# Optimization experiments

Hardware: AMD Instinct MI355X
Metric: run time of the kernel (lower is better)

The kernel has to match this reference:

```python
import jax, jax.numpy as jnp
from jax import lax
import numpy as np

BALANCE = 1.0  # polynomial kernel: (conv(x,w)+b + BALANCE)**POWER
POWER = 2


def _conv(x, w, b, stride, pad):
    y = lax.conv_general_dilated(
        x, w, window_strides=(stride, stride),
        padding=[(pad, pad), (pad, pad)],
        dimension_numbers=('NCHW', 'OIHW', 'NCHW'))
    return y + b[None, :, None, None]


def kerv2d(x, w, b, stride, pad):
    # PolyKervNets degree-2 polynomial kervolution
    y = _conv(x, w, b, stride, pad) + BALANCE
    return y * y  # (.)**2


def avgpool3s2(x):
    s = lax.reduce_window(x, 0.0, lax.add, (1, 1, 3, 3), (1, 1, 2, 2), 'VALID')
    return s * (1.0 / 9.0)


def setup_inputs() -> dict:
    key = jax.random.key(0)
    ks = jax.random.split(key, 17)
    sc = 0.01  # small init so repeated squaring stays numerically sane
    d = {}
    d['x'] = jax.random.normal(ks[0], (64, 3, 227, 227), jnp.float32)
    d['w1'] = jax.random.normal(ks[1], (96, 3, 11, 11), jnp.float32) * sc
    d['b1'] = jnp.zeros((96,), jnp.float32)
    d['w2'] = jax.random.normal(ks[2], (256, 96, 5, 5), jnp.float32) * sc
    d['b2'] = jnp.zeros((256,), jnp.float32)
    d['w3'] = jax.random.normal(ks[3], (384, 256, 3, 3), jnp.float32) * sc
    d['b3'] = jnp.zeros((384,), jnp.float32)
    d['w4'] = jax.random.normal(ks[4], (384, 384, 3, 3), jnp.float32) * sc
    d['b4'] = jnp.zeros((384,), jnp.float32)
    d['w5'] = jax.random.normal(ks[5], (256, 384, 3, 3), jnp.float32) * sc
    d['b5'] = jnp.zeros((256,), jnp.float32)
    d['fw1'] = jax.random.normal(ks[6], (9216, 4096), jnp.float32) * sc
    d['fb1'] = jnp.zeros((4096,), jnp.float32)
    d['fw2'] = jax.random.normal(ks[7], (4096, 4096), jnp.float32) * sc
    d['fb2'] = jnp.zeros((4096,), jnp.float32)
    d['fw3'] = jax.random.normal(ks[8], (4096, 1000), jnp.float32) * sc
    d['fb3'] = jnp.zeros((1000,), jnp.float32)
    return d


def reference(x, w1, b1, w2, b2, w3, b3, w4, b4, w5, b5,
              fw1, fb1, fw2, fb2, fw3, fb3):
    x = kerv2d(x, w1, b1, stride=4, pad=0)   # [B,96,55,55]
    x = avgpool3s2(x)                        # [B,96,27,27]
    x = kerv2d(x, w2, b2, stride=1, pad=2)   # [B,256,27,27]
    x = avgpool3s2(x)                        # [B,256,13,13]
    x = kerv2d(x, w3, b3, stride=1, pad=1)   # [B,384,13,13]
    x = kerv2d(x, w4, b4, stride=1, pad=1)   # [B,384,13,13]
    x = kerv2d(x, w5, b5, stride=1, pad=1)   # [B,256,13,13]
    x = avgpool3s2(x)                        # [B,256,6,6]
    x = x.reshape(x.shape[0], -1)            # [B,9216]
    x = x @ fw1 + fb1
    x = x @ fw2 + fb2
    x = x @ fw3 + fb3
    return x
```

## Files before the change

kernel.cpp:

```cpp
#include <hip/hip_runtime.h>


typedef _Float16 f16;
typedef _Float16 f16x8 __attribute__((ext_vector_type(8)));
typedef float    f32x4 __attribute__((ext_vector_type(4)));

#define CDIV(a,b) (((a)+(b)-1)/(b))
#define SWZ(row,g) ((g) ^ (((row) >> 2) & 3))

template<int C,int H,int W,int OC,int R,int S,int PAD,int STRIDE,int OH,int OW,
         int KRUN,int BM,int BN>
__global__ __launch_bounds__(256)
void conv_mfma(const f16* __restrict__ in, const f16* __restrict__ wt,
               const float* __restrict__ bias, f16* __restrict__ out)
{
    constexpr int KTOT = (KRUN > 0) ? (R * KRUN) : (C * R * S);
    constexpr int KP   = (KTOT + 31) & ~31;
    static_assert(KRUN > 0 || (C % 32) == 0, "vector path requires C % 32 == 0");
    constexpr int OHW  = OH * OW;
    constexpr int NTOT = 64 * OHW;
    constexpr int AM   = BM / 32;
    constexpr int AN   = BN / 32;
    constexpr int AU   = BM * 4 / 256;
    constexpr int BU   = BN * 4 / 256;

    __shared__ __align__(16) f16 As[BM * 32];
    __shared__ __align__(16) f16 Bs[BN * 32];

    const int t   = threadIdx.x;
    const int n0  = blockIdx.x * BN;
    const int oc0 = blockIdx.y * BM;

    int a_lds[AU]; bool a_ok[AU]; const f16* aptr[AU];
    #pragma unroll
    for (int i = 0; i < AU; ++i) {
        const int u   = t + i * 256;
        const int row = u >> 2;
        const int g   = u & 3;
        a_lds[i] = row * 32 + SWZ(row, g) * 8;
        a_ok[i]  = (oc0 + row) < OC;
        const int rowc = a_ok[i] ? (oc0 + row) : 0;
        aptr[i] = wt + (size_t)rowc * KP + g * 8;
    }
    int b_lds[BU], b_g[BU], b_img[BU], b_oy[BU], b_ox[BU]; bool b_ok[BU];
    #pragma unroll
    for (int i = 0; i < BU; ++i) {
        const int u   = t + i * 256;
        const int row = u >> 2;
        b_g[i]   = u & 3;
        b_lds[i] = row * 32 + SWZ(row, b_g[i]) * 8;
        const int n   = n0 + row;
        b_ok[i]       = n < NTOT;
        const int ncl = b_ok[i] ? n : 0;
        b_img[i] = ncl / OHW;
        const int rem = ncl - b_img[i] * OHW;
        b_oy[i]  = rem / OW;
        b_ox[i]  = rem - b_oy[i] * OW;
    }

    const int wv = t >> 6;
    const int wm = (wv >> 1) * (BM / 2);
    const int wn = (wv & 1) * (BN / 2);
    const int l  = t & 63;
    const int il = l & 15;
    const int q  = l >> 4;

    f32x4 acc[AM][AN];
    #pragma unroll
    for (int i = 0; i < AM; ++i)
        #pragma unroll
        for (int j = 0; j < AN; ++j)
            acc[i][j] = (f32x4){0.f, 0.f, 0.f, 0.f};

    int4 aReg[AU], bReg[BU];

    auto loadA = [&](int kc) {
        #pragma unroll
        for (int i = 0; i < AU; ++i) {
            int4 v = {0, 0, 0, 0};
            if (a_ok[i]) v = *(const int4*)(aptr[i] + kc);
            aReg[i] = v;
        }
    };

    const f16* bcur[BU]; bool bval[BU];
    auto setRS = [&](int r, int s) {
        if constexpr (KRUN == 0) {
            #pragma unroll
            for (int i = 0; i < BU; ++i) {
                const int iy = b_oy[i] * STRIDE + r - PAD;
                const int ix = b_ox[i] * STRIDE + s - PAD;
                bval[i] = b_ok[i] && iy >= 0 && iy < H && ix >= 0 && ix < W;
                bcur[i] = in + ((size_t)(b_img[i] * H + iy) * W + ix) * C + b_g[i] * 8;
            }
        }
    };
    auto loadBv = [&](int ccoff) {
        #pragma unroll
        for (int i = 0; i < BU; ++i) {
            int4 v = {0, 0, 0, 0};
            if (bval[i]) v = *(const int4*)(bcur[i] + ccoff);
            bReg[i] = v;
        }
    };
    auto loadB1 = [&](int kc) {
        if constexpr (KRUN > 0) {
            #pragma unroll
            for (int i = 0; i < BU; ++i) {
                const int k8 = kc + b_g[i] * 8;
                const int r  = k8 / KRUN;
                const int j0 = k8 - r * KRUN;
                int4 v = {0, 0, 0, 0};
                if (b_ok[i] && k8 < KTOT) {
                    const f16* p = in + ((size_t)(b_img[i] * H + b_oy[i] * STRIDE + r) * W
                                         + b_ox[i] * STRIDE) * C + j0;
                    const int2 lo = *(const int2*)p;
                    const int2 hi = *(const int2*)(p + 4);
                    v.x = lo.x; v.y = lo.y; v.z = hi.x; v.w = hi.y;
                }
                bReg[i] = v;
            }
        }
    };

    loadA(0);
    if constexpr (KRUN > 0) { loadB1(0); }
    else                    { setRS(0, 0); loadBv(0); }

    int rn = 0, sn = 0, ccn = 0;

    for (int kc = 0; kc < KP; kc += 32) {
        #pragma unroll
        for (int i = 0; i < AU; ++i) *(int4*)&As[a_lds[i]] = aReg[i];
        #pragma unroll
        for (int i = 0; i < BU; ++i) *(int4*)&Bs[b_lds[i]] = bReg[i];
        __syncthreads();

        if (kc + 32 < KP) {
            loadA(kc + 32);
            if constexpr (KRUN > 0) {
                loadB1(kc + 32);
            } else {
                ccn += 32;
                if (ccn == C) {
                    ccn = 0;
                    if (++sn == S) { sn = 0; ++rn; }
                    setRS(rn, sn);
                }
                loadBv(ccn);
            }
        }

        f16x8 af[AM], bf[AN];
        #pragma unroll
        for (int mi = 0; mi < AM; ++mi) {
            const int row = wm + mi * 16 + il;
            af[mi] = *(const f16x8*)&As[row * 32 + SWZ(row, q) * 8];
        }
        #pragma unroll
        for (int ni = 0; ni < AN; ++ni) {
            const int row = wn + ni * 16 + il;
            bf[ni] = *(const f16x8*)&Bs[row * 32 + SWZ(row, q) * 8];
        }
        #pragma unroll
        for (int mi = 0; mi < AM; ++mi)
            #pragma unroll
            for (int ni = 0; ni < AN; ++ni)
                acc[mi][ni] = __builtin_amdgcn_mfma_f32_16x16x32_f16(
                    af[mi], bf[ni], acc[mi][ni], 0, 0, 0);
        __syncthreads();
    }

    #pragma unroll
    for (int mi = 0; mi < AM; ++mi) {
        const int ocb = oc0 + wm + mi * 16 + q * 4;
        if (ocb >= OC) continue;
        const float4 bb = *(const float4*)(bias + ocb);
        const float b4[4] = {bb.x + 1.f, bb.y + 1.f, bb.z + 1.f, bb.w + 1.f};
        #pragma unroll
        for (int ni = 0; ni < AN; ++ni) {
            const int nn = n0 + wn + ni * 16 + il;
            if (nn >= NTOT) continue;
            const f32x4 v = acc[mi][ni];
            union { f16 h[4]; uint2 u; } cv;
            const float vv[4] = {v.x, v.y, v.z, v.w};
            #pragma unroll
            for (int rr = 0; rr < 4; ++rr) {
                const float y = vv[rr] + b4[rr];
                cv.h[rr] = (f16)(y * y);
            }
            *(uint2*)(out + (size_t)nn * OC + ocb) = cv.u;
        }
    }
}

template<bool TAIL>
__global__ __launch_bounds__(256)
void fc_mfma2(const f16* __restrict__ X, const float* __restrict__ Wm,
              float* __restrict__ P, int N, int Npad, int K, int kchunk)
{
    __shared__ __align__(16) f16 Xs[64 * 32];
    __shared__ __align__(16) f16 Ws[256 * 32];

    const int t  = threadIdx.x;
    const int n0 = blockIdx.x * 256;
    const int s  = blockIdx.y;
    const int k0 = s * kchunk;
    const int nIter = kchunk / 32;

    const bool wok = !TAIL || (n0 + t) < N;
    const float* __restrict__ wbase = Wm + (size_t)k0 * N + n0 + t;
    const int xm = t >> 2;
    const int xg = t & 3;
    const f16* __restrict__ xbase = X + (size_t)xm * K + k0 + xg * 8;
    const int xoff = xm * 32 + SWZ(xm, xg) * 8;

    const int wq = t >> 6;
    const int l  = t & 63;
    const int il = l & 15;
    const int q  = l >> 4;

    f32x4 acc[4][4];
    #pragma unroll
    for (int i = 0; i < 4; ++i)
        #pragma unroll
        for (int j = 0; j < 4; ++j)
            acc[i][j] = (f32x4){0.f, 0.f, 0.f, 0.f};

    float wreg[4][8];
    int4  xreg;

    auto loadChunk = [&](int it) {
        const size_t kbase = (size_t)it * 32;
        #pragma unroll
        for (int g = 0; g < 4; ++g)
            #pragma unroll
            for (int j = 0; j < 8; ++j)
                wreg[g][j] = wok ? wbase[(kbase + g * 8 + j) * N] : 0.f;
        xreg = *(const int4*)(xbase + kbase);
    };

    loadChunk(0);

    for (int it = 0; it < nIter; ++it) {
        #pragma unroll
        for (int g = 0; g < 4; ++g) {
            f16x8 h;
            #pragma unroll
            for (int j = 0; j < 8; ++j) h[j] = (f16)wreg[g][j];
            *(f16x8*)&Ws[t * 32 + SWZ(t, g) * 8] = h;
        }
        *(int4*)&Xs[xoff] = xreg;
        __syncthreads();

        if (it + 1 < nIter) loadChunk(it + 1);

        f16x8 af[4], bf[4];
        #pragma unroll
        for (int mi = 0; mi < 4; ++mi) {
            const int m = mi * 16 + il;
            af[mi] = *(const f16x8*)&Xs[m * 32 + SWZ(m, q) * 8];
        }
        #pragma unroll
        for (int ni = 0; ni < 4; ++ni) {
            const int n = wq * 64 + ni * 16 + il;
            bf[ni] = *(const f16x8*)&Ws[n * 32 + SWZ(n, q) * 8];
        }
        #pragma unroll
        for (int mi = 0; mi < 4; ++mi)
            #pragma unroll
            for (int ni = 0; ni < 4; ++ni)
                acc[mi][ni] = __builtin_amdgcn_mfma_f32_16x16x32_f16(
                    af[mi], bf[ni], acc[mi][ni], 0, 0, 0);
        __syncthreads();
    }

    float* __restrict__ pb = P + (size_t)s * 64 * Npad + n0;
    #pragma unroll
    for (int mi = 0; mi < 4; ++mi) {
        const int m = mi * 16 + q * 4;
        #pragma unroll
        for (int ni = 0; ni < 4; ++ni) {
            const int n = wq * 64 + ni * 16 + il;
            const f32x4 v = acc[mi][ni];
            const float vv[4] = {v.x, v.y, v.z, v.w};
            #pragma unroll
            for (int rr = 0; rr < 4; ++rr)
                pb[(size_t)(m + rr) * Npad + n] = vv[rr];
        }
    }
}

template<bool F16OUT>
__global__ __launch_bounds__(256)
void fc_reduce(const float* __restrict__ P, const float* __restrict__ bias,
               f16* __restrict__ o16, float* __restrict__ o32,
               int N, int Npad, int S)
{
    const int idx = blockIdx.x * 256 + threadIdx.x;
    const int total = 64 * (N / 4);
    if (idx >= total) return;
    const int n4 = (idx % (N / 4)) * 4;
    const int m  = idx / (N / 4);
    float4 a = *(const float4*)(bias + n4);
    const float* __restrict__ p = P + (size_t)m * Npad + n4;
    for (int s = 0; s < S; ++s) {
        const float4 v = *(const float4*)(p + (size_t)s * 64 * Npad);
        a.x += v.x; a.y += v.y; a.z += v.z; a.w += v.w;
    }
    if (F16OUT) {
        union { f16 h[4]; uint2 u; } cv;
        cv.h[0] = (f16)a.x; cv.h[1] = (f16)a.y;
        cv.h[2] = (f16)a.z; cv.h[3] = (f16)a.w;
        *(uint2*)(o16 + (size_t)m * N + n4) = cv.u;
    } else {
        *(float4*)(o32 + (size_t)m * N + n4) = a;
    }
}

__global__ __launch_bounds__(256)
void avgpool_nhwc8(const f16* __restrict__ in, f16* __restrict__ out,
                   int C8, int C, int H, int W, int OH, int OW, int total8)
{
    const int idx = blockIdx.x * 256 + threadIdx.x;
    if (idx >= total8) return;
    const int c8  = (idx % C8) * 8;
    int rest      = idx / C8;
    const int ox  = rest % OW; rest /= OW;
    const int oy  = rest % OH;
    const int b   = rest / OH;
    const f16* __restrict__ p = in + ((size_t)(b * H + oy * 2) * W + ox * 2) * C + c8;
    float s[8] = {0.f, 0.f, 0.f, 0.f, 0.f, 0.f, 0.f, 0.f};
    #pragma unroll
    for (int r = 0; r < 3; ++r)
        #pragma unroll
        for (int cc = 0; cc < 3; ++cc) {
            const f16x8 v = *(const f16x8*)&p[(r * W + cc) * C];
            #pragma unroll
            for (int j = 0; j < 8; ++j) s[j] += (float)v[j];
        }
    f16x8 o8;
    #pragma unroll
    for (int j = 0; j < 8; ++j) o8[j] = (f16)(s[j] * (1.f / 9.f));
    *(f16x8*)(out + (size_t)idx * 8) = o8;
}

__global__ __launch_bounds__(256)
void pool5_ncflat(const f16* __restrict__ in, f16* __restrict__ out)
{
    const int idx = blockIdx.x * 256 + threadIdx.x;
    if (idx >= 64 * 6 * 6 * 256) return;
    const int c  = idx & 255;
    int rest     = idx >> 8;
    const int ox = rest % 6; rest /= 6;
    const int oy = rest % 6;
    const int b  = rest / 6;
    const f16* __restrict__ p = in + ((size_t)(b * 13 + oy * 2) * 13 + ox * 2) * 256 + c;
    float s = 0.f;
    #pragma unroll
    for (int r = 0; r < 3; ++r)
        #pragma unroll
        for (int cc = 0; cc < 3; ++cc)
            s += (float)p[(r * 13 + cc) * 256];
    out[(size_t)b * 9216 + c * 36 + oy * 6 + ox] = (f16)(s * (1.f / 9.f));
}

__global__ __launch_bounds__(256)
void x_to_nhwc4(const float* __restrict__ x, f16* __restrict__ o)
{
    const int idx = blockIdx.x * 256 + threadIdx.x;
    if (idx >= 64 * 227 * 227) return;
    const int hw = idx % (227 * 227);
    const int b  = idx / (227 * 227);
    const size_t plane = 227 * 227;
    const float* __restrict__ p = x + (size_t)b * 3 * plane + hw;
    union { f16 h[4]; int2 v; } u;
    u.h[0] = (f16)p[0];
    u.h[1] = (f16)p[plane];
    u.h[2] = (f16)p[2 * plane];
    u.h[3] = (f16)0.f;
    *(int2*)(o + (size_t)idx * 4) = u.v;
}

__global__ __launch_bounds__(256)
void wt_tf1(const float* __restrict__ w, f16* __restrict__ o)
{
    const int idx = blockIdx.x * 256 + threadIdx.x;
    if (idx >= 96 * 544) return;
    const int k  = idx % 544;
    const int oc = idx / 544;
    f16 v = (f16)0.f;
    if (k < 528) {
        const int r   = k / 48;
        const int rem = k - r * 48;
        const int s   = rem >> 2;
        const int c   = rem & 3;
        if (s < 11 && c < 3)
            v = (f16)w[(((size_t)oc * 3 + c) * 11 + r) * 11 + s];
    }
    o[idx] = v;
}

__global__ __launch_bounds__(256)
void wt_tf(const float* __restrict__ w, f16* __restrict__ o,
           int OC, int Cc, int R, int S, int KP)
{
    const int idx = blockIdx.x * 256 + threadIdx.x;
    if (idx >= OC * KP) return;
    const int k  = idx % KP;
    const int oc = idx / KP;
    f16 v = (f16)0.f;
    if (k < Cc * R * S) {
        const int rs = k / Cc;
        const int c  = k - rs * Cc;
        const int r  = rs / S;
        const int s  = rs - r * S;
        v = (f16)w[(((size_t)oc * Cc + c) * R + r) * S + s];
    }
    o[idx] = v;
}

extern "C" void kernel_launch(void* const* d_in, const int* in_sizes, int n_in,
                              void* d_out, int out_size, void* d_ws, size_t ws_size,
                              hipStream_t stream)
{
    const float* x   = (const float*)d_in[0];
    const float* w1  = (const float*)d_in[1];
    const float* b1  = (const float*)d_in[2];
    const float* w2  = (const float*)d_in[3];
    const float* b2  = (const float*)d_in[4];
    const float* w3  = (const float*)d_in[5];
    const float* b3  = (const float*)d_in[6];
    const float* w4  = (const float*)d_in[7];
    const float* b4  = (const float*)d_in[8];
    const float* w5  = (const float*)d_in[9];
    const float* b5  = (const float*)d_in[10];
    const float* fw1 = (const float*)d_in[11];
    const float* fb1 = (const float*)d_in[12];
    const float* fw2 = (const float*)d_in[13];
    const float* fb2 = (const float*)d_in[14];
    const float* fw3 = (const float*)d_in[15];
    const float* fb3 = (const float*)d_in[16];
    float* out = (float*)d_out;

    char* ws = (char*)d_ws;
    const size_t MiB = 1024 * 1024;

    f16*   X0  = (f16*)(ws);
    float* P   = (float*)(ws);
    f16*   Xh1 = (f16*)(ws + 17 * MiB);
    f16*   Xh2 = (f16*)(ws + 19 * MiB);
    f16*   Xh3 = (f16*)(ws + 20 * MiB);
    f16*   A   = (f16*)(ws + 26 * MiB);
    f16*   Bp  = (f16*)(ws + 62 * MiB);
    f16*   Wt1 = (f16*)(ws + 72 * MiB);
    f16*   Wt2 = Wt1 + (size_t)96  * 544;
    f16*   Wt3 = Wt2 + (size_t)256 * 2400;
    f16*   Wt4 = Wt3 + (size_t)384 * 2304;
    f16*   Wt5 = Wt4 + (size_t)384 * 3456;

    wt_tf1<<<CDIV(96 * 544, 256), 256, 0, stream>>>(w1, Wt1);
    wt_tf<<<CDIV(256 * 2400, 256), 256, 0, stream>>>(w2, Wt2, 256, 96 , 5, 5, 2400);
    wt_tf<<<CDIV(384 * 2304, 256), 256, 0, stream>>>(w3, Wt3, 384, 256, 3, 3, 2304);
    wt_tf<<<CDIV(384 * 3456, 256), 256, 0, stream>>>(w4, Wt4, 384, 384, 3, 3, 3456);
    wt_tf<<<CDIV(256 * 3456, 256), 256, 0, stream>>>(w5, Wt5, 256, 384, 3, 3, 3456);

    x_to_nhwc4<<<CDIV(64 * 227 * 227, 256), 256, 0, stream>>>(x, X0);

    conv_mfma<4,227,227,96,11,11,0,4,55,55,48,128,128>
        <<<dim3(CDIV(64 * 55 * 55, 128), 1), 256, 0, stream>>>(X0, Wt1, b1, A);
    {
        const int total8 = 64 * 27 * 27 * (96 / 8);
        avgpool_nhwc8<<<CDIV(total8, 256), 256, 0, stream>>>(A, Bp, 96 / 8, 96, 55, 55, 27, 27, total8);
    }
    conv_mfma<96,27,27,256,5,5,2,1,27,27,0,128,128>
        <<<dim3(CDIV(64 * 27 * 27, 128), 2), 256, 0, stream>>>(Bp, Wt2, b2, A);
    {
        const int total8 = 64 * 13 * 13 * (256 / 8);
        avgpool_nhwc8<<<CDIV(total8, 256), 256, 0, stream>>>(A, Bp, 256 / 8, 256, 27, 27, 13, 13, total8);
    }
    conv_mfma<256,13,13,384,3,3,1,1,13,13,0,128,64>
        <<<dim3(169, 3), 256, 0, stream>>>(Bp, Wt3, b3, A);
    conv_mfma<384,13,13,384,3,3,1,1,13,13,0,128,64>
        <<<dim3(169, 3), 256, 0, stream>>>(A, Wt4, b4, Bp);
    conv_mfma<384,13,13,256,3,3,1,1,13,13,0,128,64>
        <<<dim3(169, 2), 256, 0, stream>>>(Bp, Wt5, b5, A);

    pool5_ncflat<<<CDIV(64 * 6 * 6 * 256, 256), 256, 0, stream>>>(A, Xh1);

    fc_mfma2<false><<<dim3(16, 16), 256, 0, stream>>>(Xh1, fw1, P, 4096, 4096, 9216, 576);
    fc_reduce<true><<<CDIV(64 * 4096 / 4, 256), 256, 0, stream>>>(P, fb1, Xh2, nullptr, 4096, 4096, 16);
    fc_mfma2<false><<<dim3(16, 16), 256, 0, stream>>>(Xh2, fw2, P, 4096, 4096, 4096, 256);
    fc_reduce<true><<<CDIV(64 * 4096 / 4, 256), 256, 0, stream>>>(P, fb2, Xh3, nullptr, 4096, 4096, 16);
    fc_mfma2<true><<<dim3(4, 64), 256, 0, stream>>>(Xh3, fw3, P, 1000, 1024, 4096, 64);
    fc_reduce<false><<<CDIV(64 * 1000 / 4, 256), 256, 0, stream>>>(P, fb3, nullptr, out, 1000, 1024, 64);
}
```

Measured before the change: 682.2 us.

## Double-buffer LDS tiles in conv and FC MFMA kernels to halve barriers

Both the conv and FC MFMA kernels now keep two shared-memory buffers. While the current chunk's fragments feed the MFMAs, the next chunk is written into the other buffer, and global loads are issued two chunks ahead. This drops one __syncthreads per iteration and overlaps the LDS stores with compute. The cost is twice the shared memory, which may reduce occupancy, plus extra register pressure from the deeper prefetch.

```diff
diff --git a/kernel.cpp b/kernel.cpp
--- a/kernel.cpp
+++ b/kernel.cpp
@@ -16,7 +16,9 @@
 {
     constexpr int KTOT = (KRUN > 0) ? (R * KRUN) : (C * R * S);
     constexpr int KP   = (KTOT + 31) & ~31;
+    constexpr int NC   = KP / 32;
     static_assert(KRUN > 0 || (C % 32) == 0, "vector path requires C % 32 == 0");
+    static_assert(NC >= 2, "double-buffer loop assumes >= 2 chunks");
     constexpr int OHW  = OH * OW;
     constexpr int NTOT = 64 * OHW;
     constexpr int AM   = BM / 32;
@@ -24,8 +26,8 @@
     constexpr int AU   = BM * 4 / 256;
     constexpr int BU   = BN * 4 / 256;
 
-    __shared__ __align__(16) f16 As[BM * 32];
-    __shared__ __align__(16) f16 Bs[BN * 32];
+    __shared__ __align__(16) f16 As[2][BM * 32];
+    __shared__ __align__(16) f16 Bs[2][BN * 32];
 
     const int t   = threadIdx.x;
     const int n0  = blockIdx.x * BN;
@@ -101,6 +103,18 @@
             int4 v = {0, 0, 0, 0};
             if (bval[i]) v = *(const int4*)(bcur[i] + ccoff);
             bReg[i] = v;
+        }
+    };
+    int rn = 0, sn = 0, ccn = 0;
+    auto advanceB = [&]() {
+        if constexpr (KRUN == 0) {
+            ccn += 32;
+            if (ccn == C) {
+                ccn = 0;
+                if (++sn == S) { sn = 0; ++rn; }
+                setRS(rn, sn);
+            }
+            loadBv(ccn);
         }
     };
     auto loadB1 = [&](int kc) {
@@ -123,52 +137,51 @@
         }
     };
 
+    auto stage = [&](int nb) {
+        #pragma unroll
+        for (int i = 0; i < AU; ++i) *(int4*)&As[nb][a_lds[i]] = aReg[i];
+        #pragma unroll
+        for (int i = 0; i < BU; ++i) *(int4*)&Bs[nb][b_lds[i]] = bReg[i];
+    };
+
     loadA(0);
-    if constexpr (KRUN > 0) { loadB1(0); }
-    else                    { setRS(0, 0); loadBv(0); }
-
-    int rn = 0, sn = 0, ccn = 0;
-
-    for (int kc = 0; kc < KP; kc += 32) {
-        #pragma unroll
-        for (int i = 0; i < AU; ++i) *(int4*)&As[a_lds[i]] = aReg[i];
-        #pragma unroll
-        for (int i = 0; i < BU; ++i) *(int4*)&Bs[b_lds[i]] = bReg[i];
-        __syncthreads();
-
-        if (kc + 32 < KP) {
-            loadA(kc + 32);
-            if constexpr (KRUN > 0) {
-                loadB1(kc + 32);
-            } else {
-                ccn += 32;
-                if (ccn == C) {
-                    ccn = 0;
-                    if (++sn == S) { sn = 0; ++rn; }
-                    setRS(rn, sn);
-                }
-                loadBv(ccn);
-            }
-        }
+    if constexpr (KRUN > 0) loadB1(0); else { setRS(0, 0); loadBv(0); }
+    stage(0);
+    loadA(32);
+    if constexpr (KRUN > 0) loadB1(32); else advanceB();
+    __syncthreads();
+
+    for (int ci = 0; ci < NC; ++ci) {
+        const int cb = ci & 1;
 
         f16x8 af[AM], bf[AN];
         #pragma unroll
         for (int mi = 0; mi < AM; ++mi) {
             const int row = wm + mi * 16 + il;
-            af[mi] = *(const f16x8*)&As[row * 32 + SWZ(row, q) * 8];
+            af[mi] = *(const f16x8*)&As[cb][row * 32 + SWZ(row, q) * 8];
         }
         #pragma unroll
         for (int ni = 0; ni < AN; ++ni) {
             const int row = wn + ni * 16 + il;
-            bf[ni] = *(const f16x8*)&Bs[row * 32 + SWZ(row, q) * 8];
-        }
+            bf[ni] = *(const f16x8*)&Bs[cb][row * 32 + SWZ(row, q) * 8];
+        }
+
+        if (ci + 1 < NC) {
+            stage(cb ^ 1);
+            if (ci + 2 < NC) {
+                loadA((ci + 2) * 32);
+                if constexpr (KRUN > 0) loadB1((ci + 2) * 32); else advanceB();
+            }
+        }
+
         #pragma unroll
         for (int mi = 0; mi < AM; ++mi)
             #pragma unroll
             for (int ni = 0; ni < AN; ++ni)
                 acc[mi][ni] = __builtin_amdgcn_mfma_f32_16x16x32_f16(
                     af[mi], bf[ni], acc[mi][ni], 0, 0, 0);
-        __syncthreads();
+
+        if (ci + 1 < NC) __syncthreads();
     }
 
     #pragma unroll
@@ -199,8 +212,8 @@
 void fc_mfma2(const f16* __restrict__ X, const float* __restrict__ Wm,
               float* __restrict__ P, int N, int Npad, int K, int kchunk)
 {
-    __shared__ __align__(16) f16 Xs[64 * 32];
-    __shared__ __align__(16) f16 Ws[256 * 32];
+    __shared__ __align__(16) f16 Xs[2][64 * 32];
+    __shared__ __align__(16) f16 Ws[2][256 * 32];
 
     const int t  = threadIdx.x;
     const int n0 = blockIdx.x * 256;
@@ -240,39 +253,50 @@
         xreg = *(const int4*)(xbase + kbase);
     };
 
-    loadChunk(0);
-
-    for (int it = 0; it < nIter; ++it) {
+    auto stage = [&](int nb) {
         #pragma unroll
         for (int g = 0; g < 4; ++g) {
             f16x8 h;
             #pragma unroll
             for (int j = 0; j < 8; ++j) h[j] = (f16)wreg[g][j];
-            *(f16x8*)&Ws[t * 32 + SWZ(t, g) * 8] = h;
-        }
-        *(int4*)&Xs[xoff] = xreg;
-        __syncthreads();
-
-        if (it + 1 < nIter) loadChunk(it + 1);
+            *(f16x8*)&Ws[nb][t * 32 + SWZ(t, g) * 8] = h;
+        }
+        *(int4*)&Xs[nb][xoff] = xreg;
+    };
+
+    loadChunk(0);
+    stage(0);
+    if (nIter > 1) loadChunk(1);
+    __syncthreads();
+
+    for (int it = 0; it < nIter; ++it) {
+        const int cb = it & 1;
 
         f16x8 af[4], bf[4];
         #pragma unroll
         for (int mi = 0; mi < 4; ++mi) {
             const int m = mi * 16 + il;
-            af[mi] = *(const f16x8*)&Xs[m * 32 + SWZ(m, q) * 8];
+            af[mi] = *(const f16x8*)&Xs[cb][m * 32 + SWZ(m, q) * 8];
         }
         #pragma unroll
         for (int ni = 0; ni < 4; ++ni) {
             const int n = wq * 64 + ni * 16 + il;
-            bf[ni] = *(const f16x8*)&Ws[n * 32 + SWZ(n, q) * 8];
-        }
+            bf[ni] = *(const f16x8*)&Ws[cb][n * 32 + SWZ(n, q) * 8];
+        }
+
+        if (it + 1 < nIter) {
+            stage(cb ^ 1);
+            if (it + 2 < nIter) loadChunk(it + 2);
+        }
+
         #pragma unroll
         for (int mi = 0; mi < 4; ++mi)
             #pragma unroll
             for (int ni = 0; ni < 4; ++ni)
                 acc[mi][ni] = __builtin_amdgcn_mfma_f32_16x16x32_f16(
                     af[mi], bf[ni], acc[mi][ni], 0, 0, 0);
-        __syncthreads();
+
+        if (it + 1 < nIter) __syncthreads();
     }
 
     float* __restrict__ pb = P + (size_t)s * 64 * Npad + n0;
```

After: 679.0 us. Within noise of the previous version (-0.5%).
